# Kernel tuning notes

Hardware: AMD Instinct MI355X
Metric: run time of the kernel (lower is better)

## Reference

```python
import jax, jax.numpy as jnp
import numpy as np

SR = 24000          # sample_rate
HOP = 256           # hop_length
K = 1024            # FIR kernel_size = nearest_power_of_two(2.2/50*24000)
RC = 512            # rnn_channels
NF = 4              # n_formants
REV = 24000         # reverb length in samples
L = HOP + K - 1     # per-frame conv output length = 1279
PI = np.pi


def _gru(x, W_ih, W_hh, b_ih, b_hh):
    # x: [B, T, H] -> [B, T, H], torch nn.GRU semantics, h0 = 0
    B = x.shape[0]

    def step(h, xt):
        gi = xt @ W_ih.T + b_ih
        gh = h @ W_hh.T + b_hh
        i_r, i_z, i_n = jnp.split(gi, 3, axis=-1)
        h_r, h_z, h_n = jnp.split(gh, 3, axis=-1)
        r = jax.nn.sigmoid(i_r + h_r)
        zg = jax.nn.sigmoid(i_z + h_z)
        n = jnp.tanh(i_n + r * h_n)
        h = (1.0 - zg) * n + zg * h
        return h, h

    h0 = jnp.zeros((B, RC), x.dtype)
    _, ys = jax.lax.scan(step, h0, jnp.swapaxes(x, 0, 1))
    return jnp.swapaxes(ys, 0, 1)


def setup_inputs() -> dict:
    key = jax.random.key(0)
    ks = jax.random.split(key, 20)
    B, F = 4, 2048
    s = 0.05
    inp = {
        'f0': jax.random.uniform(ks[0], (B, F, 1), minval=100.0, maxval=300.0),
        'loudness': jax.random.normal(ks[1], (B, F, 1)),
        'gender': jax.random.uniform(ks[2], (B, F, 2)),
        'age': jax.random.uniform(ks[3], (B, F, 8)),
        'z': jax.random.normal(ks[4], (B, F, 16)),
        'noise': jax.random.normal(ks[5], (B, F, HOP)),
        'W_in': jax.random.normal(ks[6], (RC, 28)) * s, 'b_in': jnp.zeros((RC,)),
        'W_ih': jax.random.normal(ks[7], (3 * RC, RC)) * s,
        'W_hh': jax.random.normal(ks[8], (3 * RC, RC)) * s,
        'b_ih': jnp.zeros((3 * RC,)), 'b_hh': jnp.zeros((3 * RC,)),
        'W_oq': jax.random.normal(ks[9], (1, RC)) * s, 'b_oq': jnp.zeros((1,)),
        'W_vg': jax.random.normal(ks[10], (1, RC)) * s, 'b_vg': jnp.zeros((1,)),
        'W_ug': jax.random.normal(ks[11], (1, RC)) * s, 'b_ug': jnp.zeros((1,)),
        'W_ff': jax.random.normal(ks[12], (NF, RC)) * s, 'b_ff': jnp.zeros((NF,)),
        'W_fb': jax.random.normal(ks[13], (NF, RC)) * s, 'b_fb': jnp.zeros((NF,)),
        'reverb_ir': jax.random.normal(ks[14], (REV,)) * jnp.exp(-jnp.linspace(0.0, 5.0, REV)),
        'wet_logit': jnp.float32(-1.5),
    }
    return inp


def reference(f0, loudness, gender, age, z, noise,
              W_in, b_in, W_ih, W_hh, b_ih, b_hh,
              W_oq, b_oq, W_vg, b_vg, W_ug, b_ug,
              W_ff, b_ff, W_fb, b_fb, reverb_ir, wet_logit):
    B, F, _ = f0.shape

    # ---- controller ----
    f0c = f0 - jnp.mean(f0, axis=1, keepdims=True)
    inputs = jnp.concatenate([f0c, loudness, gender, age, z], axis=-1)  # [B,F,28]
    x = jax.nn.relu(inputs @ W_in.T + b_in)
    x = _gru(x, W_ih, W_hh, b_ih, b_hh)                                  # [B,F,512]
    oq = jax.nn.sigmoid(x @ W_oq.T + b_oq)                               # [B,F,1]
    v_gain = jax.nn.softplus(x @ W_vg.T + b_vg)
    u_gain = jax.nn.softplus(x @ W_ug.T + b_ug)
    ff = jnp.cumsum(jax.nn.softplus(x @ W_ff.T + b_ff), axis=-1) + 200.0  # [B,F,4]
    fb = jax.nn.softplus(x @ W_fb.T + b_fb) + 50.0

    # ---- Rosenberg glottal source ----
    cycles = f0 * (HOP / SR)                       # [B,F,1]
    cum = jnp.cumsum(cycles, axis=1)
    start = cum - cycles
    start = start - jnp.floor(start)
    ramp = (jnp.arange(HOP, dtype=f0.dtype) / SR)[None, None, :]
    total = start + f0 * ramp                      # [B,F,HOP]
    phi = total - jnp.floor(total)
    eps = 1e-6
    peak = oq * 0.66
    rise = 0.5 * (1.0 - jnp.cos(PI * phi / (peak + eps)))
    fall = jnp.cos(PI * (phi - peak) / (2.0 * (oq - peak) + eps))
    voiced = jnp.where(phi < peak, rise, 0.0)
    voiced = jnp.where((phi >= peak) & (phi < oq), fall, voiced)

    # ---- excitation ----
    excitation = voiced * v_gain + noise * u_gain   # [B,F,HOP]

    # ---- time-varying FIR formant filter ----
    t = jnp.arange(K, dtype=f0.dtype) / SR          # [K]
    ir = jnp.exp(-PI * fb[..., None] * t) * jnp.sin(2.0 * PI * ff[..., None] * t)  # [B,F,4,K]
    combined = jnp.sum(ir, axis=2)                  # [B,F,K]
    scale = jnp.max(jnp.abs(combined), axis=-1, keepdims=True) + 1e-8
    filt = combined / scale
    # torch conv1d is cross-correlation with padding K-1 == full convolution with flipped kernel
    NFFT = 2048  # >= L = 1279, power of two
    Xf = jnp.fft.rfft(excitation, n=NFFT)
    Hf = jnp.fft.rfft(filt[..., ::-1], n=NFFT)
    conv = jnp.fft.irfft(Xf * Hf, n=NFFT)[..., :L]  # [B,F,L]

    # ---- overlap-add (F.fold) ----
    total_len = (F - 1) * HOP + L
    idx = (jnp.arange(F)[:, None] * HOP + jnp.arange(L)[None, :]).reshape(-1)
    audio = jnp.zeros((B, total_len), conv.dtype).at[:, idx].add(conv.reshape(B, -1))

    # ---- FFT reverb ----
    FFTN = 1 << 20  # >= total_len + REV - 1 = 549310
    Af = jnp.fft.rfft(audio, n=FFTN)
    Rf = jnp.fft.rfft(reverb_ir, n=FFTN)
    wetsig = jnp.fft.irfft(Af * Rf[None, :], n=FFTN)[:, :total_len]
    wet = jax.nn.sigmoid(wet_logit)
    out = ((1.0 - wet) * audio + wet * wetsig)[..., None]  # [B,total_len,1]

    return out, oq, v_gain, u_gain, ff, fb
```

## Files before the change

kernel.cpp:

```cpp
#include <hip/hip_runtime.h>
#include <hip/hip_bf16.h>
#include <math.h>

#define PI_F 3.14159265358979323846f
#define TWO_PI_F 6.283185307179586f

constexpr int BB = 4;
constexpr int FF_ = 2048;
constexpr int RC = 512;
constexpr int HOP = 256;
constexpr int KK = 1024;
constexpr int LL = HOP + KK - 1;
constexpr size_t TOT = 525311;
constexpr int APAD = 24064;
constexpr size_t AROW = 549376;
constexpr int REV = 24000;
constexpr size_t AROW2 = 551424;

constexpr size_t O1 = 2101244;
constexpr size_t O2 = 2109436;
constexpr size_t O3 = 2117628;
constexpr size_t O4 = 2125820;
constexpr size_t O5 = 2158588;

constexpr size_t OFF_X      = 0;
constexpr size_t OFF_GI     = 16777216;
constexpr size_t OFF_HS     = 67108864;
constexpr size_t OFF_OQ     = 83886080;
constexpr size_t OFF_VG     = 83918848;
constexpr size_t OFF_UG     = 83951616;
constexpr size_t OFF_FFW    = 83984384;
constexpr size_t OFF_FBW    = 84115456;
constexpr size_t OFF_START  = 84246528;
constexpr size_t OFF_F0M    = 84279296;
constexpr size_t OFF_WTAP   = 50331648;
constexpr size_t OFF_AUDIO  = 92684800;
constexpr size_t OFF_AF16   = OFF_X;

constexpr size_t OFF_HBUF   = OFF_FFW;

__device__ __forceinline__ float softplusf(float x) {
  return x > 20.0f ? x : log1pf(expf(x));
}
__device__ __forceinline__ float sigmoidf_(float x) {
  return 1.0f / (1.0f + expf(-x));
}
__device__ __forceinline__ float fastrcp(float x) {
#if __has_builtin(__builtin_amdgcn_rcpf)
  return __builtin_amdgcn_rcpf(x);
#else
  return 1.0f / x;
#endif
}

typedef _Float16 half2v __attribute__((ext_vector_type(2)));
typedef _Float16 f16x8 __attribute__((ext_vector_type(8)));
typedef float f32x4 __attribute__((ext_vector_type(4)));

__device__ __forceinline__ float dot2f(unsigned wa, unsigned hb, float acc) {
#if __has_builtin(__builtin_amdgcn_fdot2)
  union { unsigned u; half2v h; } A, B;
  A.u = wa; B.u = hb;
  return __builtin_amdgcn_fdot2(A.h, B.h, acc, false);
#else
  union { unsigned u; _Float16 h[2]; } A, B;
  A.u = wa; B.u = hb;
  return fmaf((float)A.h[0], (float)B.h[0], fmaf((float)A.h[1], (float)B.h[1], acc));
#endif
}

__global__ __launch_bounds__(256) void k_f0mean(const float* __restrict__ f0, float* __restrict__ f0m) {
  int b = blockIdx.x, tid = threadIdx.x;
  float s = 0.f;
  for (int t = tid; t < FF_; t += 256) s += f0[b*FF_ + t];
  #pragma unroll
  for (int m = 1; m < 64; m <<= 1) s += __shfl_xor(s, m);
  __shared__ float ws4[4];
  if ((tid & 63) == 0) ws4[tid >> 6] = s;
  __syncthreads();
  if (tid == 0) f0m[b] = (ws4[0] + ws4[1] + ws4[2] + ws4[3]) * (1.0f / 2048.0f);
}

__global__ __launch_bounds__(256) void k_inproj(
    const float* __restrict__ f0, const float* __restrict__ loud,
    const float* __restrict__ gender, const float* __restrict__ age,
    const float* __restrict__ z, const float* __restrict__ f0m,
    const float* __restrict__ Win, const float* __restrict__ bin,
    float* __restrict__ x)
{
  __shared__ float inp[16 * 28];
  int r0 = blockIdx.x * 16;
  int tid = threadIdx.x;
  for (int i = tid; i < 16 * 28; i += 256) {
    int r = i / 28, c = i % 28;
    int bf = r0 + r, b = bf >> 11;
    float v;
    if (c == 0)       v = f0[bf] - f0m[b];
    else if (c == 1)  v = loud[bf];
    else if (c < 4)   v = gender[(size_t)bf*2 + (c - 2)];
    else if (c < 12)  v = age[(size_t)bf*8 + (c - 4)];
    else              v = z[(size_t)bf*16 + (c - 12)];
    inp[i] = v;
  }
  __syncthreads();
  for (int o = tid; o < 16 * 512; o += 256) {
    int r = o >> 9, j = o & 511;
    const float* w = Win + j * 28;
    const float* ip = inp + r * 28;
    float a = bin[j];
    #pragma unroll
    for (int c2 = 0; c2 < 28; ++c2) a = fmaf(w[c2], ip[c2], a);
    x[(size_t)(r0 + r) * 512 + j] = fmaxf(a, 0.0f);
  }
}

__global__ __launch_bounds__(256) void k_gemm_gi(
    const float* __restrict__ A, const float* __restrict__ Bw,
    const float* __restrict__ bias, float* __restrict__ C)
{
  __shared__ unsigned As[64 * 20];
  __shared__ unsigned Bs[64 * 20];
  int tid = threadIdx.x;
  int n0 = blockIdx.x * 64, m0 = blockIdx.y * 64;
  const int w = tid >> 6;
  const int lane = tid & 63;
  const int mrow0 = (w >> 1) * 32;
  const int ncol0 = (w & 1) * 32;
  const int lm = lane & 15;
  const int quad = lane >> 4;

  f32x4 acc00 = {0.f,0.f,0.f,0.f}, acc01 = {0.f,0.f,0.f,0.f};
  f32x4 acc10 = {0.f,0.f,0.f,0.f}, acc11 = {0.f,0.f,0.f,0.f};

  for (int k0 = 0; k0 < 512; k0 += 32) {
    __syncthreads();
    for (int i = tid; i < 1024; i += 256) {
      int r = i >> 4, d = i & 15;
      float2 av = *(const float2*)(A + (size_t)(m0 + r) * 512 + k0 + 2 * d);
      float2 bv = *(const float2*)(Bw + (size_t)(n0 + r) * 512 + k0 + 2 * d);
      union { unsigned u32; _Float16 h[2]; } pa, pb;
      pa.h[0] = (_Float16)av.x; pa.h[1] = (_Float16)av.y;
      pb.h[0] = (_Float16)bv.x; pb.h[1] = (_Float16)bv.y;
      As[r * 20 + d] = pa.u32;
      Bs[r * 20 + d] = pb.u32;
    }
    __syncthreads();
    union { uint4 u; f16x8 h; } a0, a1, b0, b1;
    a0.u = *(const uint4*)&As[(mrow0 + lm) * 20 + quad * 4];
    a1.u = *(const uint4*)&As[(mrow0 + 16 + lm) * 20 + quad * 4];
    b0.u = *(const uint4*)&Bs[(ncol0 + lm) * 20 + quad * 4];
    b1.u = *(const uint4*)&Bs[(ncol0 + 16 + lm) * 20 + quad * 4];
    acc00 = __builtin_amdgcn_mfma_f32_16x16x32_f16(a0.h, b0.h, acc00, 0, 0, 0);
    acc01 = __builtin_amdgcn_mfma_f32_16x16x32_f16(a0.h, b1.h, acc01, 0, 0, 0);
    acc10 = __builtin_amdgcn_mfma_f32_16x16x32_f16(a1.h, b0.h, acc10, 0, 0, 0);
    acc11 = __builtin_amdgcn_mfma_f32_16x16x32_f16(a1.h, b1.h, acc11, 0, 0, 0);
  }
  #pragma unroll
  for (int sm = 0; sm < 2; ++sm) {
    #pragma unroll
    for (int sn = 0; sn < 2; ++sn) {
      const f32x4& ac = sm ? (sn ? acc11 : acc10) : (sn ? acc01 : acc00);
      int col = n0 + ncol0 + sn * 16 + lm;
      float bb = bias[col];
      #pragma unroll
      for (int rg = 0; rg < 4; ++rg) {
        int row = m0 + mrow0 + sm * 16 + quad * 4 + rg;
        C[(size_t)row * 1536 + col] = ac[rg] + bb;
      }
    }
  }
}

__global__ __launch_bounds__(256, 1) void k_gru(
    const float* __restrict__ Whh, const float* __restrict__ bhh,
    const float* __restrict__ gi, float* __restrict__ hs,
    unsigned long long* hbuf)
{
  __shared__ unsigned hs2[2][292];
  __shared__ float red[2][384];
  __shared__ float bhh_s[48];

  const int tid = threadIdx.x;
  const int bid = blockIdx.x;
  const int b   = (bid & 7) >> 1;
  const int wgi = ((bid >> 3) << 1) | (bid & 1);
  const int u0  = wgi * 16;
  const int piece = tid & 7;
  const int rp    = tid >> 3;

  unsigned w0r[32], w1r[32];
  if (tid < 192) {
    int r0 = 2 * rp, r1 = 2 * rp + 1;
    const float* s0 = Whh + (size_t)((r0 >> 4) * 512 + u0 + (r0 & 15)) * 512 + piece * 64;
    const float* s1 = Whh + (size_t)((r1 >> 4) * 512 + u0 + (r1 & 15)) * 512 + piece * 64;
    #pragma unroll
    for (int j = 0; j < 32; ++j) {
      float2 a = *(const float2*)(s0 + 2 * j);
      float2 c = *(const float2*)(s1 + 2 * j);
      union { unsigned u32; _Float16 hh[2]; } ca, cb;
      ca.hh[0] = (_Float16)a.x; ca.hh[1] = (_Float16)a.y;
      cb.hh[0] = (_Float16)c.x; cb.hh[1] = (_Float16)c.y;
      w0r[j] = ca.u32; w1r[j] = cb.u32;
    }
  } else {
    #pragma unroll
    for (int j = 0; j < 32; ++j) { w0r[j] = 0u; w1r[j] = 0u; }
  }
  if (tid < 48) bhh_s[tid] = bhh[(tid >> 4) * 512 + u0 + (tid & 15)];
  __syncthreads();

  float hprev = 0.0f;

  #pragma unroll 1
  for (unsigned t = 0; t < 2048; ++t) {
    const int p = (int)(t & 1u);
    float gir = 0.f, giz = 0.f, gin = 0.f;
    if (tid < 16) {
      const float* gp = gi + (size_t)(b * 2048 + (int)t) * 1536 + u0 + tid;
      gir = gp[0]; giz = gp[512]; gin = gp[1024];
    }
    {
      const unsigned long long* pp = hbuf + ((size_t)p * 4 + b) * 256 + tid;
      unsigned long long w = __hip_atomic_load(pp, __ATOMIC_RELAXED, __HIP_MEMORY_SCOPE_AGENT);
      while ((unsigned)(w >> 32) != t)
        w = __hip_atomic_load(pp, __ATOMIC_RELAXED, __HIP_MEMORY_SCOPE_AGENT);
      hs2[p][(tid >> 5) * 36 + (tid & 31)] = (unsigned)w;
    }
    __syncthreads();
    if (tid < 192) {
      const unsigned* hp = &hs2[p][piece * 36];
      float a00 = 0.f, a01 = 0.f, a10 = 0.f, a11 = 0.f;
      #pragma unroll
      for (int i = 0; i < 8; ++i) {
        uint4 h4 = *(const uint4*)(hp + 4 * i);
        a00 = dot2f(w0r[4 * i + 0], h4.x, a00);
        a01 = dot2f(w0r[4 * i + 1], h4.y, a01);
        a00 = dot2f(w0r[4 * i + 2], h4.z, a00);
        a01 = dot2f(w0r[4 * i + 3], h4.w, a01);
        a10 = dot2f(w1r[4 * i + 0], h4.x, a10);
        a11 = dot2f(w1r[4 * i + 1], h4.y, a11);
        a10 = dot2f(w1r[4 * i + 2], h4.z, a10);
        a11 = dot2f(w1r[4 * i + 3], h4.w, a11);
      }
      red[p][(2 * rp) * 8 + piece]     = a00 + a01;
      red[p][(2 * rp + 1) * 8 + piece] = a10 + a11;
    }
    __syncthreads();
    if (tid < 16) {
      const float* r0p = &red[p][tid * 8];
      const float* r1p = &red[p][(16 + tid) * 8];
      const float* r2p = &red[p][(32 + tid) * 8];
      float4 q0 = *(const float4*)r0p, q1 = *(const float4*)(r0p + 4);
      float4 z0 = *(const float4*)r1p, z1 = *(const float4*)(r1p + 4);
      float4 n0 = *(const float4*)r2p, n1 = *(const float4*)(r2p + 4);
      float ghr = ((q0.x + q0.y) + (q0.z + q0.w)) + ((q1.x + q1.y) + (q1.z + q1.w)) + bhh_s[tid];
      float ghz = ((z0.x + z0.y) + (z0.z + z0.w)) + ((z1.x + z1.y) + (z1.z + z1.w)) + bhh_s[16 + tid];
      float ghn = ((n0.x + n0.y) + (n0.z + n0.w)) + ((n1.x + n1.y) + (n1.z + n1.w)) + bhh_s[32 + tid];
      float r  = fastrcp(1.0f + __expf(-(gir + ghr)));
      float zg = fastrcp(1.0f + __expf(-(giz + ghz)));
      float e2 = __expf(2.0f * (gin + r * ghn));
      float n  = 1.0f - 2.0f * fastrcp(e2 + 1.0f);
      float hnew = (1.0f - zg) * n + zg * hprev;
      hprev = hnew;
      float hpart = __shfl_xor(hnew, 1);
      if ((tid & 1) == 0) {
        union { unsigned u32; _Float16 hh[2]; } pk;
        pk.hh[0] = (_Float16)hnew;
        pk.hh[1] = (_Float16)hpart;
        unsigned long long wq = ((unsigned long long)(t + 1u) << 32) | (unsigned long long)pk.u32;
        __hip_atomic_store(hbuf + ((size_t)((t + 1u) & 1u) * 4 + b) * 256 + (u0 >> 1) + (tid >> 1),
                           wq, __ATOMIC_RELAXED, __HIP_MEMORY_SCOPE_AGENT);
      }
      hs[(size_t)(b * 2048 + (int)t) * 512 + u0 + tid] = hnew;
    }
  }
}

__global__ __launch_bounds__(256) void k_heads(
    const float* __restrict__ hs,
    const float* __restrict__ Woq, const float* __restrict__ boq,
    const float* __restrict__ Wvg, const float* __restrict__ bvg,
    const float* __restrict__ Wug, const float* __restrict__ bug,
    const float* __restrict__ Wff, const float* __restrict__ bff,
    const float* __restrict__ Wfb, const float* __restrict__ bfb,
    float* __restrict__ out,
    float* __restrict__ oqw, float* __restrict__ vgw, float* __restrict__ ugw,
    float* __restrict__ ffw, float* __restrict__ fbw)
{
  int bf = blockIdx.x, tid = threadIdx.x;
  const float* h = hs + (size_t)bf * 512;
  float p[11];
  #pragma unroll
  for (int i = 0; i < 11; ++i) p[i] = 0.f;
  for (int k = tid; k < 512; k += 256) {
    float hv = h[k];
    p[0] = fmaf(Woq[k], hv, p[0]);
    p[1] = fmaf(Wvg[k], hv, p[1]);
    p[2] = fmaf(Wug[k], hv, p[2]);
    p[3] = fmaf(Wff[k], hv, p[3]);
    p[4] = fmaf(Wff[512 + k], hv, p[4]);
    p[5] = fmaf(Wff[1024 + k], hv, p[5]);
    p[6] = fmaf(Wff[1536 + k], hv, p[6]);
    p[7] = fmaf(Wfb[k], hv, p[7]);
    p[8] = fmaf(Wfb[512 + k], hv, p[8]);
    p[9] = fmaf(Wfb[1024 + k], hv, p[9]);
    p[10] = fmaf(Wfb[1536 + k], hv, p[10]);
  }
  #pragma unroll
  for (int i = 0; i < 11; ++i) {
    float v = p[i];
    #pragma unroll
    for (int m = 1; m < 64; m <<= 1) v += __shfl_xor(v, m);
    p[i] = v;
  }
  __shared__ float r4[4][11];
  if ((tid & 63) == 0) {
    int w = tid >> 6;
    #pragma unroll
    for (int i = 0; i < 11; ++i) r4[w][i] = p[i];
  }
  __syncthreads();
  if (tid == 0) {
    float s[11];
    #pragma unroll
    for (int i = 0; i < 11; ++i) s[i] = r4[0][i] + r4[1][i] + r4[2][i] + r4[3][i];
    float oqv = sigmoidf_(s[0] + boq[0]);
    float vg = softplusf(s[1] + bvg[0]);
    float ug = softplusf(s[2] + bug[0]);
    out[O1 + bf] = oqv; oqw[bf] = oqv;
    out[O2 + bf] = vg;  vgw[bf] = vg;
    out[O3 + bf] = ug;  ugw[bf] = ug;
    float run = 200.0f;
    #pragma unroll
    for (int j = 0; j < 4; ++j) {
      run += softplusf(s[3 + j] + bff[j]);
      out[O4 + (size_t)bf * 4 + j] = run; ffw[(size_t)bf * 4 + j] = run;
    }
    #pragma unroll
    for (int j = 0; j < 4; ++j) {
      float g = softplusf(s[7 + j] + bfb[j]) + 50.0f;
      out[O5 + (size_t)bf * 4 + j] = g; fbw[(size_t)bf * 4 + j] = g;
    }
  }
}

__global__ __launch_bounds__(256) void k_scan(const float* __restrict__ f0, float* __restrict__ startw) {
  __shared__ float ts[256];
  int b = blockIdx.x, tid = threadIdx.x;
  const float CY = 256.0f / 24000.0f;
  float c[8], run = 0.f;
  int base = b * 2048 + tid * 8;
  #pragma unroll
  for (int j = 0; j < 8; ++j) { c[j] = run; run += f0[base + j] * CY; }
  ts[tid] = run;
  __syncthreads();
  for (int off = 1; off < 256; off <<= 1) {
    float v = (tid >= off) ? ts[tid - off] : 0.0f;
    __syncthreads();
    ts[tid] += v;
    __syncthreads();
  }
  float excl = (tid == 0) ? 0.0f : ts[tid - 1];
  #pragma unroll
  for (int j = 0; j < 8; ++j) {
    float st = excl + c[j];
    startw[base + j] = st - floorf(st);
  }
}

__global__ __launch_bounds__(256) void k_synth(
    const float* __restrict__ f0, const float* __restrict__ noise,
    const float* __restrict__ startw, const float* __restrict__ oqw,
    const float* __restrict__ vgw, const float* __restrict__ ugw,
    const float* __restrict__ ffw, const float* __restrict__ fbw,
    float* __restrict__ audio)
{
  __shared__ float es[256];
  __shared__ float fp[1536];
  __shared__ float ffs[4], fbs[4], ssc[1], wmax[4];
  int bf = blockIdx.x, tid = threadIdx.x;
  int b = bf >> 11, f = bf & 2047;

  {
    float st = startw[bf], f0v = f0[bf], oqv = oqw[bf], vg = vgw[bf], ug = ugw[bf];
    float total = st + f0v * ((float)tid * (1.0f / 24000.0f));
    float phi = total - floorf(total);
    float peak = oqv * 0.66f;
    float rise = 0.5f * (1.0f - __cosf(PI_F * phi / (peak + 1e-6f)));
    float fall = __cosf(PI_F * (phi - peak) / (2.0f * (oqv - peak) + 1e-6f));
    float v = (phi < peak) ? rise : ((phi < oqv) ? fall : 0.0f);
    es[tid] = v * vg + noise[(size_t)bf * 256 + tid] * ug;
  }
  if (tid < 4) { ffs[tid] = ffw[(size_t)bf * 4 + tid]; fbs[tid] = fbw[(size_t)bf * 4 + tid]; }
  fp[tid] = 0.0f;
  fp[1280 + tid] = 0.0f;
  __syncthreads();

  float vals[4];
  float am = 0.f;
  #pragma unroll
  for (int it = 0; it < 4; ++it) {
    int k = it * 256 + tid;
    float t = (float)k * (1.0f / 24000.0f);
    float s = 0.f;
    #pragma unroll
    for (int j = 0; j < 4; ++j)
      s += __expf(-PI_F * fbs[j] * t) * __sinf(TWO_PI_F * ffs[j] * t);
    vals[it] = s;
    am = fmaxf(am, fabsf(s));
  }
  #pragma unroll
  for (int m = 1; m < 64; m <<= 1) am = fmaxf(am, __shfl_xor(am, m));
  if ((tid & 63) == 0) wmax[tid >> 6] = am;
  __syncthreads();
  if (tid == 0) ssc[0] = fmaxf(fmaxf(wmax[0], wmax[1]), fmaxf(wmax[2], wmax[3])) + 1e-8f;
  __syncthreads();
  float inv = 1.0f / ssc[0];
  #pragma unroll
  for (int it = 0; it < 4; ++it) {
    int k = it * 256 + tid;
    fp[256 + (1023 - k)] = vals[it] * inv;
  }
  __syncthreads();

  int n0 = tid * 5;
  float V0 = fp[n0 + 256], V1 = fp[n0 + 257], V2 = fp[n0 + 258], V3 = fp[n0 + 259], V4 = fp[n0 + 260];
  float a0 = 0.f, a1 = 0.f, a2 = 0.f, a3 = 0.f, a4 = 0.f;
  #pragma unroll 4
  for (int m = 0; m < 256; ++m) {
    float e = es[m];
    a0 = fmaf(e, V0, a0); a1 = fmaf(e, V1, a1); a2 = fmaf(e, V2, a2);
    a3 = fmaf(e, V3, a3); a4 = fmaf(e, V4, a4);
    V4 = V3; V3 = V2; V2 = V1; V1 = V0;
    V0 = fp[n0 + 255 - m];
  }
  float* arow = audio + (size_t)b * AROW + APAD + (size_t)f * 256;
  if (n0 + 0 < LL) atomicAdd(&arow[n0 + 0], a0);
  if (n0 + 1 < LL) atomicAdd(&arow[n0 + 1], a1);
  if (n0 + 2 < LL) atomicAdd(&arow[n0 + 2], a2);
  if (n0 + 3 < LL) atomicAdd(&arow[n0 + 3], a3);
  if (n0 + 4 < LL) atomicAdd(&arow[n0 + 4], a4);
}

__global__ __launch_bounds__(256) void k_packaudio(const float* __restrict__ audio,
                                                   unsigned* __restrict__ af) {
  int idx = blockIdx.x * 256 + threadIdx.x;
  int b = blockIdx.y;
  size_t i0 = (size_t)idx * 2;
  if (i0 < AROW2) {
    float a = (i0 < AROW)     ? audio[(size_t)b * AROW + i0]     : 0.0f;
    float c = (i0 + 1 < AROW) ? audio[(size_t)b * AROW + i0 + 1] : 0.0f;
    union { unsigned u32; _Float16 h[2]; } pk;
    pk.h[0] = (_Float16)a; pk.h[1] = (_Float16)c;
    af[(size_t)b * (AROW2 / 2) + idx] = pk.u32;
  }
}

__global__ __launch_bounds__(256) void k_wtaps(const float* __restrict__ ir, uint4* __restrict__ wtap) {
  int g = blockIdx.x * 256 + threadIdx.x;
  int p = g >> 6, l = g & 63;
  if (p < 752) {
    int base = 32 * p + 16 + (l & 15) - ((l >> 4) << 3);
    unsigned dw[4];
    #pragma unroll
    for (int j = 0; j < 4; ++j) {
      int i0 = base - 2 * j, i1 = base - 2 * j - 1;
      float v0 = (i0 >= 0 && i0 < REV) ? ir[i0] : 0.0f;
      float v1 = (i1 >= 0 && i1 < REV) ? ir[i1] : 0.0f;
      union { unsigned u32; _Float16 h[2]; } pk;
      pk.h[0] = (_Float16)v0; pk.h[1] = (_Float16)v1;
      dw[j] = pk.u32;
    }
    uint4 o; o.x = dw[0]; o.y = dw[1]; o.z = dw[2]; o.w = dw[3];
    wtap[(size_t)(p << 6) + l] = o;
  }
}

constexpr int PC = 16;
constexpr int NCHUNK = 47;
constexpr int WINH = 2544;

__global__ __launch_bounds__(256) void k_reverb(
    const float* __restrict__ audio, const unsigned short* __restrict__ af,
    const uint4* __restrict__ wtap, const float* __restrict__ wetl,
    float* __restrict__ out)
{
  __shared__ __align__(16) unsigned short win[WINH];
  __shared__ uint4 wlds[PC * 64];
  int tb = blockIdx.x, b = blockIdx.y, tid = threadIdx.x;
  const int wv = tid >> 6, lane = tid & 63;
  const int lm = lane & 15, quad = lane >> 4;
  int q0 = tb * 128;
  const unsigned short* afrow = af + (size_t)b * AROW2;
  f32x4 acc0 = {0.f,0.f,0.f,0.f}, acc1 = {0.f,0.f,0.f,0.f};

  for (int c = 0; c < NCHUNK; ++c) {
    int p0 = c * PC;
    int b_lo = 16 * q0 - 32 * (p0 + PC - 1) - 16;
    const uint4* src = (const uint4*)(afrow + (APAD + b_lo));
    __syncthreads();
    for (int u = tid; u < 318 + PC * 64; u += 256) {
      if (u < 318) ((uint4*)win)[u] = src[u];
      else         wlds[u - 318] = wtap[(size_t)p0 * 64 + (u - 318)];
    }
    __syncthreads();
    int offb = 16 * lm + 8 * quad;
    int tA = (2 * wv) * 256 + offb, tB = (2 * wv + 1) * 256 + offb;
    #pragma unroll 4
    for (int pl = 0; pl < PC; ++pl) {
      union { uint4 u; f16x8 h; } wf, b0, b1;
      wf.u = wlds[pl * 64 + lane];
      int offp = 32 * (PC - 1 - pl);
      b0.u = *(const uint4*)&win[offp + tA];
      b1.u = *(const uint4*)&win[offp + tB];
      acc0 = __builtin_amdgcn_mfma_f32_16x16x32_f16(wf.h, b0.h, acc0, 0, 0, 0);
      acc1 = __builtin_amdgcn_mfma_f32_16x16x32_f16(wf.h, b1.h, acc1, 0, 0, 0);
    }
  }
  float wet = sigmoidf_(wetl[0]);
  const float* arow = audio + (size_t)b * AROW;
  #pragma unroll
  for (int tile = 0; tile < 2; ++tile) {
    const f32x4& ac = tile ? acc1 : acc0;
    int qt = q0 + (2 * wv + tile) * 16 + lm;
    #pragma unroll
    for (int rg = 0; rg < 4; ++rg) {
      long t = (long)16 * qt + quad * 4 + rg;
      if (t < (long)TOT) {
        float av = arow[APAD + t];
        out[(size_t)b * TOT + t] = (1.0f - wet) * av + wet * ac[rg];
      }
    }
  }
}

extern "C" void kernel_launch(void* const* d_in, const int* in_sizes, int n_in,
                              void* d_out, int out_size, void* d_ws, size_t ws_size,
                              hipStream_t stream) {
  const float* f0       = (const float*)d_in[0];
  const float* loud     = (const float*)d_in[1];
  const float* gender   = (const float*)d_in[2];
  const float* age      = (const float*)d_in[3];
  const float* z        = (const float*)d_in[4];
  const float* noise    = (const float*)d_in[5];
  const float* W_in     = (const float*)d_in[6];
  const float* b_in     = (const float*)d_in[7];
  const float* W_ih     = (const float*)d_in[8];
  const float* W_hh     = (const float*)d_in[9];
  const float* b_ih     = (const float*)d_in[10];
  const float* b_hh     = (const float*)d_in[11];
  const float* W_oq     = (const float*)d_in[12];
  const float* b_oq     = (const float*)d_in[13];
  const float* W_vg     = (const float*)d_in[14];
  const float* b_vg     = (const float*)d_in[15];
  const float* W_ug     = (const float*)d_in[16];
  const float* b_ug     = (const float*)d_in[17];
  const float* W_ff     = (const float*)d_in[18];
  const float* b_ff     = (const float*)d_in[19];
  const float* W_fb     = (const float*)d_in[20];
  const float* b_fb     = (const float*)d_in[21];
  const float* rev_ir   = (const float*)d_in[22];
  const float* wet_l    = (const float*)d_in[23];

  float* out = (float*)d_out;
  char* ws = (char*)d_ws;
  float* x      = (float*)(ws + OFF_X);
  float* gi     = (float*)(ws + OFF_GI);
  float* hs     = (float*)(ws + OFF_HS);
  float* oqw    = (float*)(ws + OFF_OQ);
  float* vgw    = (float*)(ws + OFF_VG);
  float* ugw    = (float*)(ws + OFF_UG);
  float* ffw    = (float*)(ws + OFF_FFW);
  float* fbw    = (float*)(ws + OFF_FBW);
  float* startw = (float*)(ws + OFF_START);
  float* f0m    = (float*)(ws + OFF_F0M);
  unsigned long long* hbuf = (unsigned long long*)(ws + OFF_HBUF);
  uint4* wtap   = (uint4*)(ws + OFF_WTAP);
  unsigned* af  = (unsigned*)(ws + OFF_AF16);
  float* audio  = (float*)(ws + OFF_AUDIO);

  hipMemsetAsync(ws + OFF_HBUF, 0, 16384, stream);
  hipMemsetAsync(ws + OFF_AUDIO, 0, (size_t)4 * AROW * 4, stream);

  k_f0mean<<<4, 256, 0, stream>>>(f0, f0m);
  k_inproj<<<512, 256, 0, stream>>>(f0, loud, gender, age, z, f0m, W_in, b_in, x);
  k_gemm_gi<<<dim3(24, 128), 256, 0, stream>>>(x, W_ih, b_ih, gi);
  k_gru<<<128, 256, 0, stream>>>(W_hh, b_hh, gi, hs, hbuf);
  k_heads<<<8192, 256, 0, stream>>>(hs, W_oq, b_oq, W_vg, b_vg, W_ug, b_ug,
                                    W_ff, b_ff, W_fb, b_fb, out, oqw, vgw, ugw, ffw, fbw);
  k_scan<<<4, 256, 0, stream>>>(f0, startw);
  k_wtaps<<<188, 256, 0, stream>>>(rev_ir, wtap);
  k_synth<<<8192, 256, 0, stream>>>(f0, noise, startw, oqw, vgw, ugw, ffw, fbw, audio);
  k_packaudio<<<dim3(1077, 4), 256, 0, stream>>>(audio, af);
  k_reverb<<<dim3(257, 4), 256, 0, stream>>>(audio, (const unsigned short*)af, wtap, wet_l, out);
}
```

Baseline: 3.278 ms.

## Halve GRU persistent blocks by giving each block 32 hidden units

The persistent GRU kernel now launches 64 blocks instead of 128, and each block owns 32 hidden units instead of 16. Each thread holds twice as many fp16-packed recurrent weights in registers and covers 128 columns instead of 64, with a 4-way rather than 8-way partial-sum reduction. The goal is to cut the number of blocks taking part in the per-timestep cross-block handoff, lowering synchronization and polling overhead on the serial recurrence. The cost is twice the dot-product work per thread per step and higher register pressure, which could lengthen the critical path of each step.

```diff
diff --git a/kernel.cpp b/kernel.cpp
--- a/kernel.cpp
+++ b/kernel.cpp
@@ -178,23 +178,23 @@
 {
   __shared__ unsigned hs2[2][292];
   __shared__ float red[2][384];
-  __shared__ float bhh_s[48];
+  __shared__ float bhh_s[96];
 
   const int tid = threadIdx.x;
   const int bid = blockIdx.x;
   const int b   = (bid & 7) >> 1;
   const int wgi = ((bid >> 3) << 1) | (bid & 1);
-  const int u0  = wgi * 16;
-  const int piece = tid & 7;
-  const int rp    = tid >> 3;
-
-  unsigned w0r[32], w1r[32];
+  const int u0  = wgi * 32;
+  const int piece = tid & 3;
+  const int rp    = tid >> 2;
+
+  unsigned w0r[64], w1r[64];
   if (tid < 192) {
     int r0 = 2 * rp, r1 = 2 * rp + 1;
-    const float* s0 = Whh + (size_t)((r0 >> 4) * 512 + u0 + (r0 & 15)) * 512 + piece * 64;
-    const float* s1 = Whh + (size_t)((r1 >> 4) * 512 + u0 + (r1 & 15)) * 512 + piece * 64;
-    #pragma unroll
-    for (int j = 0; j < 32; ++j) {
+    const float* s0 = Whh + (size_t)((r0 >> 5) * 512 + u0 + (r0 & 31)) * 512 + piece * 128;
+    const float* s1 = Whh + (size_t)((r1 >> 5) * 512 + u0 + (r1 & 31)) * 512 + piece * 128;
+    #pragma unroll
+    for (int j = 0; j < 64; ++j) {
       float2 a = *(const float2*)(s0 + 2 * j);
       float2 c = *(const float2*)(s1 + 2 * j);
       union { unsigned u32; _Float16 hh[2]; } ca, cb;
@@ -204,9 +204,9 @@
     }
   } else {
     #pragma unroll
-    for (int j = 0; j < 32; ++j) { w0r[j] = 0u; w1r[j] = 0u; }
-  }
-  if (tid < 48) bhh_s[tid] = bhh[(tid >> 4) * 512 + u0 + (tid & 15)];
+    for (int j = 0; j < 64; ++j) { w0r[j] = 0u; w1r[j] = 0u; }
+  }
+  if (tid < 96) bhh_s[tid] = bhh[(tid >> 5) * 512 + u0 + (tid & 31)];
   __syncthreads();
 
   float hprev = 0.0f;
@@ -215,7 +215,7 @@
   for (unsigned t = 0; t < 2048; ++t) {
     const int p = (int)(t & 1u);
     float gir = 0.f, giz = 0.f, gin = 0.f;
-    if (tid < 16) {
+    if (tid < 32) {
       const float* gp = gi + (size_t)(b * 2048 + (int)t) * 1536 + u0 + tid;
       gir = gp[0]; giz = gp[512]; gin = gp[1024];
     }
@@ -228,11 +228,12 @@
     }
     __syncthreads();
     if (tid < 192) {
-      const unsigned* hp = &hs2[p][piece * 36];
+      const unsigned* hp0 = &hs2[p][(2 * piece) * 36];
+      const unsigned* hp1 = &hs2[p][(2 * piece + 1) * 36];
       float a00 = 0.f, a01 = 0.f, a10 = 0.f, a11 = 0.f;
       #pragma unroll
       for (int i = 0; i < 8; ++i) {
-        uint4 h4 = *(const uint4*)(hp + 4 * i);
+        uint4 h4 = *(const uint4*)(hp0 + 4 * i);
         a00 = dot2f(w0r[4 * i + 0], h4.x, a00);
         a01 = dot2f(w0r[4 * i + 1], h4.y, a01);
         a00 = dot2f(w0r[4 * i + 2], h4.z, a00);
@@ -242,20 +243,29 @@
         a10 = dot2f(w1r[4 * i + 2], h4.z, a10);
         a11 = dot2f(w1r[4 * i + 3], h4.w, a11);
       }
-      red[p][(2 * rp) * 8 + piece]     = a00 + a01;
-      red[p][(2 * rp + 1) * 8 + piece] = a10 + a11;
-    }
-    __syncthreads();
-    if (tid < 16) {
-      const float* r0p = &red[p][tid * 8];
-      const float* r1p = &red[p][(16 + tid) * 8];
-      const float* r2p = &red[p][(32 + tid) * 8];
-      float4 q0 = *(const float4*)r0p, q1 = *(const float4*)(r0p + 4);
-      float4 z0 = *(const float4*)r1p, z1 = *(const float4*)(r1p + 4);
-      float4 n0 = *(const float4*)r2p, n1 = *(const float4*)(r2p + 4);
-      float ghr = ((q0.x + q0.y) + (q0.z + q0.w)) + ((q1.x + q1.y) + (q1.z + q1.w)) + bhh_s[tid];
-      float ghz = ((z0.x + z0.y) + (z0.z + z0.w)) + ((z1.x + z1.y) + (z1.z + z1.w)) + bhh_s[16 + tid];
-      float ghn = ((n0.x + n0.y) + (n0.z + n0.w)) + ((n1.x + n1.y) + (n1.z + n1.w)) + bhh_s[32 + tid];
+      #pragma unroll
+      for (int i = 0; i < 8; ++i) {
+        uint4 h4 = *(const uint4*)(hp1 + 4 * i);
+        a00 = dot2f(w0r[32 + 4 * i + 0], h4.x, a00);
+        a01 = dot2f(w0r[32 + 4 * i + 1], h4.y, a01);
+        a00 = dot2f(w0r[32 + 4 * i + 2], h4.z, a00);
+        a01 = dot2f(w0r[32 + 4 * i + 3], h4.w, a01);
+        a10 = dot2f(w1r[32 + 4 * i + 0], h4.x, a10);
+        a11 = dot2f(w1r[32 + 4 * i + 1], h4.y, a11);
+        a10 = dot2f(w1r[32 + 4 * i + 2], h4.z, a10);
+        a11 = dot2f(w1r[32 + 4 * i + 3], h4.w, a11);
+      }
+      red[p][(2 * rp) * 4 + piece]     = a00 + a01;
+      red[p][(2 * rp + 1) * 4 + piece] = a10 + a11;
+    }
+    __syncthreads();
+    if (tid < 32) {
+      float4 q0 = *(const float4*)&red[p][tid * 4];
+      float4 z0 = *(const float4*)&red[p][(32 + tid) * 4];
+      float4 n0 = *(const float4*)&red[p][(64 + tid) * 4];
+      float ghr = ((q0.x + q0.y) + (q0.z + q0.w)) + bhh_s[tid];
+      float ghz = ((z0.x + z0.y) + (z0.z + z0.w)) + bhh_s[32 + tid];
+      float ghn = ((n0.x + n0.y) + (n0.z + n0.w)) + bhh_s[64 + tid];
       float r  = fastrcp(1.0f + __expf(-(gir + ghr)));
       float zg = fastrcp(1.0f + __expf(-(giz + ghz)));
       float e2 = __expf(2.0f * (gin + r * ghn));
@@ -585,7 +595,7 @@
   k_f0mean<<<4, 256, 0, stream>>>(f0, f0m);
   k_inproj<<<512, 256, 0, stream>>>(f0, loud, gender, age, z, f0m, W_in, b_in, x);
   k_gemm_gi<<<dim3(24, 128), 256, 0, stream>>>(x, W_ih, b_ih, gi);
-  k_gru<<<128, 256, 0, stream>>>(W_hh, b_hh, gi, hs, hbuf);
+  k_gru<<<64, 256, 0, stream>>>(W_hh, b_hh, gi, hs, hbuf);
   k_heads<<<8192, 256, 0, stream>>>(hs, W_oq, b_oq, W_vg, b_vg, W_ug, b_ug,
                                     W_ff, b_ff, W_fb, b_fb, out, oqw, vgw, ugw, ffw, fbw);
   k_scan<<<4, 256, 0, stream>>>(f0, startw);
```

After: 3.237 ms. No clear change (-1.3%).
